# Kernel tuning notes

Measured on AMD Instinct MI355X. Metric: run time of the kernel, lower is better.

The kernel has to match this reference:

```python
import jax, jax.numpy as jnp
import numpy as np

N_NODES = 100000
N_EDGES = 1600000
D = 128            # in_size == d_model == 128
N_LAYERS = 4
N_GRAPHS = 64
N_CLASS = 10
BN_EPS = 1e-5


def setup_inputs() -> dict:
    key = jax.random.key(0)
    ks = jax.random.split(key, 20)
    x = jax.random.normal(ks[0], (N_NODES, D), dtype=jnp.float32)
    edge_index = jax.random.randint(ks[1], (2, N_EDGES), 0, N_NODES, dtype=jnp.int32)
    batch = jnp.sort(jax.random.randint(ks[2], (N_NODES,), 0, N_GRAPHS, dtype=jnp.int32))
    s = 0.05
    # stacked per-layer GINConv MLP params (all layers are D->D since in_size==d_model)
    W1 = jax.random.normal(ks[3], (N_LAYERS, D, D), dtype=jnp.float32) * s
    b1 = jnp.zeros((N_LAYERS, D), dtype=jnp.float32)
    W2 = jax.random.normal(ks[4], (N_LAYERS, D, D), dtype=jnp.float32) * s
    b2 = jnp.zeros((N_LAYERS, D), dtype=jnp.float32)
    gamma = jnp.ones((N_LAYERS, D), dtype=jnp.float32)
    beta = jnp.zeros((N_LAYERS, D), dtype=jnp.float32)
    eps = jnp.zeros((N_LAYERS,), dtype=jnp.float32)  # train_eps=True, init 0
    fcw1 = jax.random.normal(ks[5], (D, D), dtype=jnp.float32) * s
    fcb1 = jnp.zeros((D,), dtype=jnp.float32)
    fcw2 = jax.random.normal(ks[6], (D, D // 2), dtype=jnp.float32) * s
    fcb2 = jnp.zeros((D // 2,), dtype=jnp.float32)
    fcw3 = jax.random.normal(ks[7], (D // 2, N_CLASS), dtype=jnp.float32) * s
    fcb3 = jnp.zeros((N_CLASS,), dtype=jnp.float32)
    return dict(x=x, edge_index=edge_index, batch=batch, W1=W1, b1=b1, W2=W2, b2=b2,
                gamma=gamma, beta=beta, eps=eps, fcw1=fcw1, fcb1=fcb1,
                fcw2=fcw2, fcb2=fcb2, fcw3=fcw3, fcb3=fcb3)


def _batchnorm(z, g, b):
    # BatchNorm1d in training mode: batch stats over nodes, biased variance
    m = jnp.mean(z, axis=0)
    v = jnp.var(z, axis=0)
    return g * (z - m) * jax.lax.rsqrt(v + BN_EPS) + b


def reference(x, edge_index, batch, W1, b1, W2, b2, gamma, beta, eps,
              fcw1, fcb1, fcw2, fcb2, fcw3, fcb3):
    # StandardScaler: per-feature standardization over all nodes (ddof=0)
    mu = jnp.mean(x, axis=0)
    sd = jnp.sqrt(jnp.var(x, axis=0))
    h = (x - mu) / sd
    src, dst = edge_index[0], edge_index[1]
    for l in range(N_LAYERS):
        # GINConv: MLP((1+eps)*x_i + sum_{j in N(i)} x_j)
        agg = jax.ops.segment_sum(h[src], dst, num_segments=N_NODES)
        z = (1.0 + eps[l]) * h + agg
        z = jax.nn.relu(z @ W1[l] + b1[l])
        z = jax.nn.relu(z @ W2[l] + b2[l])
        z = _batchnorm(z, gamma[l], beta[l])
        h = jax.nn.relu(z)  # outer F.relu in forward
    g = jax.ops.segment_sum(h, batch, num_segments=N_GRAPHS)  # global_add_pool
    g = jax.nn.relu(g @ fcw1 + fcb1)   # dropout omitted (eval/deterministic)
    g = jax.nn.relu(g @ fcw2 + fcb2)
    return g @ fcw3 + fcb3
```

## Files before the change

kernel.cpp:

```cpp
#include <hip/hip_runtime.h>
#include <hip/hip_bf16.h>
#include <math.h>

#define N_NODES 100000
#define N_EDGES 1600000
#define D 128
#define N_LAYERS 4
#define N_GRAPHS 64
#define N_CLASS 10
#define BN_EPS 1e-5f

#define POOL_ROWS 128
#define LDK 136

#define EB_CHUNK 4096
#define EDGE_BLOCKS ((N_EDGES + EB_CHUNK - 1) / EB_CHUNK)
#define NPB 512
#define NB ((N_NODES + NPB - 1) / NPB)

typedef __attribute__((ext_vector_type(8))) short bf16x8;
typedef __attribute__((ext_vector_type(4))) float f32x4;

__device__ inline float b2f(ushort u) {
    return __builtin_bit_cast(float, (unsigned)u << 16);
}
__device__ inline ushort f2b(float f) {
    unsigned u = __builtin_bit_cast(unsigned, f);
    return (ushort)((u + 0x7fffu + ((u >> 16) & 1u)) >> 16);
}

__global__ void zero_u32_kernel(unsigned int* __restrict__ p, int n) {
    int i = blockIdx.x * blockDim.x + threadIdx.x;
    if (i < n) p[i] = 0u;
}


__global__ void bucket_count_kernel(const int* __restrict__ dst, int* __restrict__ bucketCount) {
    __shared__ int bc[NB];
    int tid = threadIdx.x;
    if (tid < NB) bc[tid] = 0;
    __syncthreads();
    int base = blockIdx.x * EB_CHUNK;
#pragma unroll
    for (int i = 0; i < 16; ++i) {
        int e = base + i * 256 + tid;
        if (e < N_EDGES) atomicAdd(&bc[dst[e] >> 9], 1);
    }
    __syncthreads();
    if (tid < NB && bc[tid]) atomicAdd(&bucketCount[tid], bc[tid]);
}

__global__ void bucket_scan_kernel(const int* __restrict__ bucketCount,
                                   int* __restrict__ bucketBase, int* __restrict__ bucketCursor) {
    __shared__ int lds[256];
    int tid = threadIdx.x;
    int v = (tid < NB) ? bucketCount[tid] : 0;
    lds[tid] = v;
    __syncthreads();
    for (int off = 1; off < 256; off <<= 1) {
        int x = (tid >= off) ? lds[tid - off] : 0;
        __syncthreads();
        lds[tid] += x;
        __syncthreads();
    }
    int excl = lds[tid] - v;
    if (tid < NB) { bucketBase[tid] = excl; bucketCursor[tid] = excl; }
    if (tid == NB - 1) bucketBase[NB] = excl + v;
}

__global__ void bucket_scatter_kernel(const int* __restrict__ src, const int* __restrict__ dst,
                                      int* __restrict__ bucketCursor, int2* __restrict__ bpairs) {
    __shared__ int lcnt[NB];
    int tid = threadIdx.x;
    if (tid < NB) lcnt[tid] = 0;
    __syncthreads();
    int base = blockIdx.x * EB_CHUNK;
    int s[16], d[16];
#pragma unroll
    for (int i = 0; i < 16; ++i) {
        int e = base + i * 256 + tid;
        if (e < N_EDGES) {
            s[i] = src[e]; d[i] = dst[e];
            atomicAdd(&lcnt[d[i] >> 9], 1);
        } else {
            d[i] = -1;
        }
    }
    __syncthreads();
    if (tid < NB) {
        int c = lcnt[tid];
        lcnt[tid] = c ? atomicAdd(&bucketCursor[tid], c) : 0;
    }
    __syncthreads();
#pragma unroll
    for (int i = 0; i < 16; ++i) {
        if (d[i] >= 0) {
            int p = atomicAdd(&lcnt[d[i] >> 9], 1);
            bpairs[p] = make_int2(s[i], d[i]);
        }
    }
}

__launch_bounds__(512)
__global__ void csr_build_kernel(const int2* __restrict__ bpairs, const int* __restrict__ bucketBase,
                                 int* __restrict__ rowptr, int* __restrict__ colidx) {
    __shared__ int cnt[NPB];
    __shared__ int cur[NPB];
    int tid = threadIdx.x;
    int b = blockIdx.x;
    int nb0 = b * NPB;
    int ebase = bucketBase[b];
    int eend = bucketBase[b + 1];
    cnt[tid] = 0;
    __syncthreads();
    for (int e = ebase + tid; e < eend; e += 512)
        atomicAdd(&cnt[bpairs[e].y - nb0], 1);
    __syncthreads();
    int v = cnt[tid];
    for (int off = 1; off < 512; off <<= 1) {
        int x = (tid >= off) ? cnt[tid - off] : 0;
        __syncthreads();
        cnt[tid] += x;
        __syncthreads();
    }
    int excl = cnt[tid] - v;
    int node = nb0 + tid;
    if (node < N_NODES) rowptr[node] = ebase + excl;
    cur[tid] = ebase + excl;
    __syncthreads();
    for (int e = ebase + tid; e < eend; e += 512) {
        int2 pr = bpairs[e];
        int p = atomicAdd(&cur[pr.y - nb0], 1);
        colidx[p] = pr.x;
    }
    if (b == 0 && tid == 0) rowptr[N_NODES] = N_EDGES;
}

__global__ void colstats_kernel(const float* __restrict__ x, float* __restrict__ stats) {
    __shared__ float ssum[D];
    __shared__ float ssq[D];
    int tid = threadIdx.x;
    if (tid < D) { ssum[tid] = 0.f; ssq[tid] = 0.f; }
    __syncthreads();
    int f4 = (tid & 31) * 4;
    int rsub = tid >> 5;
    int r0 = blockIdx.x * 128;
    int rend = r0 + 128;
    if (rend > N_NODES) rend = N_NODES;
    float4 ps = make_float4(0.f, 0.f, 0.f, 0.f);
    float4 pq = make_float4(0.f, 0.f, 0.f, 0.f);
    for (int r = r0 + rsub; r < rend; r += 8) {
        float4 v = *(const float4*)&x[(size_t)r * D + f4];
        ps.x += v.x; ps.y += v.y; ps.z += v.z; ps.w += v.w;
        pq.x += v.x * v.x; pq.y += v.y * v.y; pq.z += v.z * v.z; pq.w += v.w * v.w;
    }
    atomicAdd(&ssum[f4 + 0], ps.x); atomicAdd(&ssum[f4 + 1], ps.y);
    atomicAdd(&ssum[f4 + 2], ps.z); atomicAdd(&ssum[f4 + 3], ps.w);
    atomicAdd(&ssq[f4 + 0], pq.x);  atomicAdd(&ssq[f4 + 1], pq.y);
    atomicAdd(&ssq[f4 + 2], pq.z);  atomicAdd(&ssq[f4 + 3], pq.w);
    __syncthreads();
    if (tid < D) {
        atomicAdd(&stats[tid], ssum[tid]);
        atomicAdd(&stats[D + tid], ssq[tid]);
    }
}

__global__ void standardize_kernel(const float* __restrict__ x, const float* __restrict__ stats,
                                   ushort* __restrict__ h) {
    const float invN = 1.f / (float)N_NODES;
    int stride = gridDim.x * blockDim.x;
    const int total = N_NODES * (D / 4);
    for (int idx = blockIdx.x * blockDim.x + threadIdx.x; idx < total; idx += stride) {
        int f = (idx & 31) * 4;
        float4 v = ((const float4*)x)[idx];
        float o[4];
        float vv[4] = {v.x, v.y, v.z, v.w};
#pragma unroll
        for (int j = 0; j < 4; ++j) {
            float mu = stats[f + j] * invN;
            float sd = sqrtf(stats[D + f + j] * invN - mu * mu);
            o[j] = (vv[j] - mu) / sd;
        }
        ((ushort4*)h)[idx] = make_ushort4(f2b(o[0]), f2b(o[1]), f2b(o[2]), f2b(o[3]));
    }
}

__global__ void agg_kernel(const ushort* __restrict__ h, const int* __restrict__ rowptr,
                           const int* __restrict__ colidx, const float* __restrict__ eps, int l,
                           const float* __restrict__ ab, int relu_flag,
                           ushort* __restrict__ z0) {
    int node = blockIdx.x * 8 + (threadIdx.x >> 5);
    int f4 = (threadIdx.x & 31) * 4;
    const ushort* hp = h + f4;
    float A0 = ab[f4 + 0], A1 = ab[f4 + 1], A2 = ab[f4 + 2], A3 = ab[f4 + 3];
    float B0 = ab[D + f4 + 0], B1 = ab[D + f4 + 1], B2 = ab[D + f4 + 2], B3 = ab[D + f4 + 3];
    float lo = relu_flag ? 0.f : -INFINITY;

    ushort4 c = *(const ushort4*)&hp[(size_t)node * D];
    float se = 1.f + eps[l];
    float ax = se * fmaxf(fmaf(b2f(c.x), A0, B0), lo);
    float ay = se * fmaxf(fmaf(b2f(c.y), A1, B1), lo);
    float az = se * fmaxf(fmaf(b2f(c.z), A2, B2), lo);
    float aw = se * fmaxf(fmaf(b2f(c.w), A3, B3), lo);

    int e = rowptr[node], e1 = rowptr[node + 1];
    for (; e + 2 <= e1; e += 2) {
        int s0 = colidx[e];
        int s1 = colidx[e + 1];
        ushort4 v0 = *(const ushort4*)&hp[(size_t)s0 * D];
        ushort4 v1 = *(const ushort4*)&hp[(size_t)s1 * D];
        ax += fmaxf(fmaf(b2f(v0.x), A0, B0), lo) + fmaxf(fmaf(b2f(v1.x), A0, B0), lo);
        ay += fmaxf(fmaf(b2f(v0.y), A1, B1), lo) + fmaxf(fmaf(b2f(v1.y), A1, B1), lo);
        az += fmaxf(fmaf(b2f(v0.z), A2, B2), lo) + fmaxf(fmaf(b2f(v1.z), A2, B2), lo);
        aw += fmaxf(fmaf(b2f(v0.w), A3, B3), lo) + fmaxf(fmaf(b2f(v1.w), A3, B3), lo);
    }
    if (e < e1) {
        int s0 = colidx[e];
        ushort4 v0 = *(const ushort4*)&hp[(size_t)s0 * D];
        ax += fmaxf(fmaf(b2f(v0.x), A0, B0), lo);
        ay += fmaxf(fmaf(b2f(v0.y), A1, B1), lo);
        az += fmaxf(fmaf(b2f(v0.z), A2, B2), lo);
        aw += fmaxf(fmaf(b2f(v0.w), A3, B3), lo);
    }
    *(ushort4*)&z0[(size_t)node * D + f4] = make_ushort4(f2b(ax), f2b(ay), f2b(az), f2b(aw));
}

__global__ void prep_wt_kernel(const float* __restrict__ W1, const float* __restrict__ W2,
                               ushort* __restrict__ wt) {
    int idx = blockIdx.x * blockDim.x + threadIdx.x;
    int w = idx >> 16;
    int rem = idx & 65535;
    int l = rem >> 14;
    int nk = rem & 16383;
    int n = nk >> 7;
    int k = nk & 127;
    const float* W = w ? W2 : W1;
    wt[idx] = f2b(W[((size_t)(l * D + k)) * D + n]);
}

__launch_bounds__(256, 2)
__global__ void mlp_mfma_kernel(const ushort* __restrict__ z0,
                                const ushort* __restrict__ wt1, const float* __restrict__ b1,
                                const ushort* __restrict__ wt2, const float* __restrict__ b2,
                                ushort* __restrict__ out, float* __restrict__ stats) {
    __shared__ ushort As[128 * LDK];
    __shared__ ushort Bs[128 * LDK];
    __shared__ float Ssum[D];
    __shared__ float Ssq[D];

    int tid = threadIdx.x;
    int lane = tid & 63;
    int wave = tid >> 6;
    int rb = blockIdx.x * 128;
    int lrow = lane & 15;
    int lk = lane >> 4;
    int klane = lk * 8;
    int wr0 = wave * 32;

    if (tid < D) { Ssum[tid] = 0.f; Ssq[tid] = 0.f; }

#pragma unroll
    for (int i = 0; i < 8; ++i) {
        int c2 = tid + i * 256;
        int row = c2 >> 4;
        int cc = (c2 & 15) * 8;
        int gr = rb + row;
        bf16x8 v;
#pragma unroll
        for (int e = 0; e < 8; ++e) v[e] = 0;
        if (gr < N_NODES) v = *(const bf16x8*)&z0[(size_t)gr * D + cc];
        *(bf16x8*)&As[row * LDK + cc] = v;
        *(bf16x8*)&Bs[row * LDK + cc] = *(const bf16x8*)&wt1[c2 * 8];
    }
    __syncthreads();

    f32x4 acc[2][8];
#pragma unroll
    for (int a = 0; a < 2; ++a)
#pragma unroll
        for (int b = 0; b < 8; ++b)
#pragma unroll
            for (int r = 0; r < 4; ++r) acc[a][b][r] = 0.f;

#pragma unroll
    for (int ks = 0; ks < 4; ++ks) {
        int k0 = ks * 32 + klane;
        bf16x8 a0 = *(const bf16x8*)&As[(wr0 + lrow) * LDK + k0];
        bf16x8 a1 = *(const bf16x8*)&As[(wr0 + 16 + lrow) * LDK + k0];
#pragma unroll
        for (int ct = 0; ct < 8; ++ct) {
            bf16x8 bb = *(const bf16x8*)&Bs[(ct * 16 + lrow) * LDK + k0];
            acc[0][ct] = __builtin_amdgcn_mfma_f32_16x16x32_bf16(a0, bb, acc[0][ct], 0, 0, 0);
            acc[1][ct] = __builtin_amdgcn_mfma_f32_16x16x32_bf16(a1, bb, acc[1][ct], 0, 0, 0);
        }
    }
    __syncthreads();

#pragma unroll
    for (int rt = 0; rt < 2; ++rt)
#pragma unroll
        for (int ct = 0; ct < 8; ++ct) {
            int col = ct * 16 + lrow;
            float bias = b1[col];
#pragma unroll
            for (int r = 0; r < 4; ++r) {
                int row = wr0 + rt * 16 + lk * 4 + r;
                As[row * LDK + col] = f2b(fmaxf(acc[rt][ct][r] + bias, 0.f));
            }
        }
#pragma unroll
    for (int i = 0; i < 8; ++i) {
        int c2 = tid + i * 256;
        int row = c2 >> 4;
        int cc = (c2 & 15) * 8;
        *(bf16x8*)&Bs[row * LDK + cc] = *(const bf16x8*)&wt2[c2 * 8];
    }
#pragma unroll
    for (int a = 0; a < 2; ++a)
#pragma unroll
        for (int b = 0; b < 8; ++b)
#pragma unroll
            for (int r = 0; r < 4; ++r) acc[a][b][r] = 0.f;
    __syncthreads();

#pragma unroll
    for (int ks = 0; ks < 4; ++ks) {
        int k0 = ks * 32 + klane;
        bf16x8 a0 = *(const bf16x8*)&As[(wr0 + lrow) * LDK + k0];
        bf16x8 a1 = *(const bf16x8*)&As[(wr0 + 16 + lrow) * LDK + k0];
#pragma unroll
        for (int ct = 0; ct < 8; ++ct) {
            bf16x8 bb = *(const bf16x8*)&Bs[(ct * 16 + lrow) * LDK + k0];
            acc[0][ct] = __builtin_amdgcn_mfma_f32_16x16x32_bf16(a0, bb, acc[0][ct], 0, 0, 0);
            acc[1][ct] = __builtin_amdgcn_mfma_f32_16x16x32_bf16(a1, bb, acc[1][ct], 0, 0, 0);
        }
    }
    __syncthreads();

#pragma unroll
    for (int rt = 0; rt < 2; ++rt)
#pragma unroll
        for (int ct = 0; ct < 8; ++ct) {
            int col = ct * 16 + lrow;
            float bias = b2[col];
            float s = 0.f, sq = 0.f;
#pragma unroll
            for (int r = 0; r < 4; ++r) {
                int row = wr0 + rt * 16 + lk * 4 + r;
                float v = fmaxf(acc[rt][ct][r] + bias, 0.f);
                Bs[row * LDK + col] = f2b(v);
                if (rb + row < N_NODES) { s += v; sq += v * v; }
            }
            atomicAdd(&Ssum[col], s);
            atomicAdd(&Ssq[col], sq);
        }
    __syncthreads();

#pragma unroll
    for (int i = 0; i < 8; ++i) {
        int c2 = tid + i * 256;
        int row = c2 >> 4;
        int cc = (c2 & 15) * 8;
        int gr = rb + row;
        if (gr < N_NODES)
            *(bf16x8*)&out[(size_t)gr * D + cc] = *(const bf16x8*)&Bs[row * LDK + cc];
    }
    if (tid < D) {
        atomicAdd(&stats[tid], Ssum[tid]);
        atomicAdd(&stats[D + tid], Ssq[tid]);
    }
}

__global__ void bnprep_kernel(const float* __restrict__ stats, const float* __restrict__ gamma,
                              const float* __restrict__ beta, float* __restrict__ ab) {
    int f = threadIdx.x;
    if (f < D) {
        const float invN = 1.f / (float)N_NODES;
        float mu = stats[f] * invN;
        float var = stats[D + f] * invN - mu * mu;
        float A = gamma[f] * rsqrtf(var + BN_EPS);
        ab[f] = A;
        ab[D + f] = beta[f] - mu * A;
    }
}

__global__ void init_ab_kernel(float* __restrict__ ab) {
    int f = threadIdx.x;
    if (f < D) { ab[f] = 1.f; ab[D + f] = 0.f; }
}

__global__ void pool_kernel(const ushort* __restrict__ h, const int* __restrict__ batch,
                            const float* __restrict__ ab, float* __restrict__ g) {
    int tid = threadIdx.x;
    int f4 = (tid & 31) * 4;
    int rsub = tid >> 5;
    int r0 = blockIdx.x * POOL_ROWS;
    int rend = r0 + POOL_ROWS;
    if (rend > N_NODES) rend = N_NODES;
    float A0 = ab[f4 + 0], A1 = ab[f4 + 1], A2 = ab[f4 + 2], A3 = ab[f4 + 3];
    float B0 = ab[D + f4 + 0], B1 = ab[D + f4 + 1], B2 = ab[D + f4 + 2], B3 = ab[D + f4 + 3];
    float4 acc = make_float4(0.f, 0.f, 0.f, 0.f);
    int cur = -1;
    for (int r = r0 + rsub; r < rend; r += 8) {
        int b = batch[r];
        if (b != cur) {
            if (cur >= 0) {
                atomicAdd(&g[cur * D + f4 + 0], acc.x);
                atomicAdd(&g[cur * D + f4 + 1], acc.y);
                atomicAdd(&g[cur * D + f4 + 2], acc.z);
                atomicAdd(&g[cur * D + f4 + 3], acc.w);
            }
            acc = make_float4(0.f, 0.f, 0.f, 0.f);
            cur = b;
        }
        ushort4 v = *(const ushort4*)&h[(size_t)r * D + f4];
        acc.x += fmaxf(fmaf(b2f(v.x), A0, B0), 0.f);
        acc.y += fmaxf(fmaf(b2f(v.y), A1, B1), 0.f);
        acc.z += fmaxf(fmaf(b2f(v.z), A2, B2), 0.f);
        acc.w += fmaxf(fmaf(b2f(v.w), A3, B3), 0.f);
    }
    if (cur >= 0) {
        atomicAdd(&g[cur * D + f4 + 0], acc.x);
        atomicAdd(&g[cur * D + f4 + 1], acc.y);
        atomicAdd(&g[cur * D + f4 + 2], acc.z);
        atomicAdd(&g[cur * D + f4 + 3], acc.w);
    }
}

__launch_bounds__(512)
__global__ void head_kernel(const float* __restrict__ g,
                            const float* __restrict__ fcw1, const float* __restrict__ fcb1,
                            const float* __restrict__ fcw2, const float* __restrict__ fcb2,
                            const float* __restrict__ fcw3, const float* __restrict__ fcb3,
                            float* __restrict__ out) {
    __shared__ float G[64][128];
    __shared__ float T1[64][128];
    __shared__ float T2[64][64];
    int tid = threadIdx.x;
#pragma unroll
    for (int i = 0; i < 4; ++i) {
        int slot = tid + i * 512;
        ((float4*)G)[slot] = ((const float4*)g)[slot];
    }
    __syncthreads();
#pragma unroll 1
    for (int rep = 0; rep < 16; ++rep) {
        int o = tid + rep * 512;
        int r = o >> 7, c = o & 127;
        float acc = fcb1[c];
        for (int k = 0; k < 128; ++k) acc = fmaf(G[r][k], fcw1[k * 128 + c], acc);
        T1[r][c] = fmaxf(acc, 0.f);
    }
    __syncthreads();
#pragma unroll 1
    for (int rep = 0; rep < 8; ++rep) {
        int o = tid + rep * 512;
        int r = o >> 6, c = o & 63;
        float acc = fcb2[c];
        for (int k = 0; k < 128; ++k) acc = fmaf(T1[r][k], fcw2[k * 64 + c], acc);
        T2[r][c] = fmaxf(acc, 0.f);
    }
    __syncthreads();
    for (int o = tid; o < N_GRAPHS * N_CLASS; o += 512) {
        int r = o / 10, c = o % 10;
        float acc = fcb3[c];
        for (int k = 0; k < 64; ++k) acc = fmaf(T2[r][k], fcw3[k * 10 + c], acc);
        out[o] = acc;
    }
}

extern "C" void kernel_launch(void* const* d_in, const int* in_sizes, int n_in,
                              void* d_out, int out_size, void* d_ws, size_t ws_size,
                              hipStream_t stream) {
    const float* x        = (const float*)d_in[0];
    const int* edge_index = (const int*)d_in[1];
    const int* batch      = (const int*)d_in[2];
    const float* W1       = (const float*)d_in[3];
    const float* b1       = (const float*)d_in[4];
    const float* W2       = (const float*)d_in[5];
    const float* b2       = (const float*)d_in[6];
    const float* gamma    = (const float*)d_in[7];
    const float* beta     = (const float*)d_in[8];
    const float* eps      = (const float*)d_in[9];
    const float* fcw1     = (const float*)d_in[10];
    const float* fcb1     = (const float*)d_in[11];
    const float* fcw2     = (const float*)d_in[12];
    const float* fcb2     = (const float*)d_in[13];
    const float* fcw3     = (const float*)d_in[14];
    const float* fcb3     = (const float*)d_in[15];
    float* out = (float*)d_out;

    char* ws = (char*)d_ws;
    size_t off = 0;
    auto alloc = [&](size_t bytes) -> void* {
        void* p = ws + off;
        off = (off + bytes + 255) & ~(size_t)255;
        return p;
    };
    ushort* hbuf   = (ushort*)alloc((size_t)N_NODES * D * 2);
    ushort* z0buf  = (ushort*)alloc((size_t)N_NODES * D * 2);
    ushort* wtbuf  = (ushort*)alloc((size_t)2 * N_LAYERS * D * D * 2);
    int2* bpairs   = (int2*)alloc((size_t)N_EDGES * 8);
    int* colidx    = (int*)alloc((size_t)N_EDGES * 4);
    int* rowptr    = (int*)alloc((size_t)(N_NODES + 1) * 4);
    int* bucketCount  = (int*)alloc((size_t)NB * 4);
    int* bucketBase   = (int*)alloc((size_t)(NB + 1) * 4);
    int* bucketCursor = (int*)alloc((size_t)NB * 4);
    float* stats   = (float*)alloc(4 * D * 4);
    float* gpool   = (float*)alloc((size_t)N_GRAPHS * D * 4);
    float* ab      = stats + 2 * D;

    const int* srcArr = edge_index;
    const int* dstArr = edge_index + N_EDGES;

    zero_u32_kernel<<<1, 256, 0, stream>>>((unsigned int*)bucketCount, NB);
    bucket_count_kernel<<<EDGE_BLOCKS, 256, 0, stream>>>(dstArr, bucketCount);
    bucket_scan_kernel<<<1, 256, 0, stream>>>(bucketCount, bucketBase, bucketCursor);
    bucket_scatter_kernel<<<EDGE_BLOCKS, 256, 0, stream>>>(srcArr, dstArr, bucketCursor, bpairs);
    csr_build_kernel<<<NB, 512, 0, stream>>>(bpairs, bucketBase, rowptr, colidx);

    zero_u32_kernel<<<1, 256, 0, stream>>>((unsigned int*)stats, 2 * D);
    colstats_kernel<<<(N_NODES + 127) / 128, 256, 0, stream>>>(x, stats);
    standardize_kernel<<<2048, 256, 0, stream>>>(x, stats, hbuf);

    prep_wt_kernel<<<512, 256, 0, stream>>>(W1, W2, wtbuf);
    init_ab_kernel<<<1, 128, 0, stream>>>(ab);

    for (int l = 0; l < N_LAYERS; ++l) {
        agg_kernel<<<N_NODES / 8, 256, 0, stream>>>(hbuf, rowptr, colidx, eps, l,
                                                    ab, (l > 0) ? 1 : 0, z0buf);
        zero_u32_kernel<<<1, 256, 0, stream>>>((unsigned int*)stats, 2 * D);
        mlp_mfma_kernel<<<(N_NODES + 127) / 128, 256, 0, stream>>>(
            z0buf, wtbuf + (size_t)l * D * D, b1 + (size_t)l * D,
            wtbuf + (size_t)(N_LAYERS + l) * D * D, b2 + (size_t)l * D, hbuf, stats);
        bnprep_kernel<<<1, 128, 0, stream>>>(stats, gamma + (size_t)l * D,
                                             beta + (size_t)l * D, ab);
    }

    zero_u32_kernel<<<(N_GRAPHS * D + 255) / 256, 256, 0, stream>>>((unsigned int*)gpool, N_GRAPHS * D);
    pool_kernel<<<(N_NODES + POOL_ROWS - 1) / POOL_ROWS, 256, 0, stream>>>(hbuf, batch, ab, gpool);
    head_kernel<<<1, 512, 0, stream>>>(gpool, fcw1, fcb1, fcw2, fcb2, fcw3, fcb3, out);
}
```

Measured before the change: 851.4 us.

## Split node features into 16-wide channel planes for cache-local gather aggregation

Stores node features in 8 channel-major planes of 16 bf16 values each, and has the aggregation kernel process one plane per block, with the plane chosen by block index. Each plane is small enough to stay resident in a cache slice, which is meant to cut DRAM traffic from the random neighbor gathers. The standardize, MLP load/store and pool kernels are adapted to the new layout. The tradeoff is narrower 4-byte gathers per thread and repeated reads of rowptr and colidx across the 8 planes.

```diff
diff --git a/kernel.cpp b/kernel.cpp
--- a/kernel.cpp
+++ b/kernel.cpp
@@ -13,6 +13,10 @@
 #define POOL_ROWS 128
 #define LDK 136
 
+#define NCH 8
+#define CHF 16
+#define CH_STRIDE ((size_t)N_NODES * CHF)
+
 #define EB_CHUNK 4096
 #define EDGE_BLOCKS ((N_EDGES + EB_CHUNK - 1) / EB_CHUNK)
 #define NPB 512
@@ -33,7 +37,6 @@
     int i = blockIdx.x * blockDim.x + threadIdx.x;
     if (i < n) p[i] = 0u;
 }
-
 
 __global__ void bucket_count_kernel(const int* __restrict__ dst, int* __restrict__ bucketCount) {
     __shared__ int bc[NB];
@@ -169,10 +172,14 @@
                                    ushort* __restrict__ h) {
     const float invN = 1.f / (float)N_NODES;
     int stride = gridDim.x * blockDim.x;
-    const int total = N_NODES * (D / 4);
+    const int total = NCH * N_NODES * 4;
     for (int idx = blockIdx.x * blockDim.x + threadIdx.x; idx < total; idx += stride) {
-        int f = (idx & 31) * 4;
-        float4 v = ((const float4*)x)[idx];
+        int c = idx / (N_NODES * 4);
+        int rem = idx - c * (N_NODES * 4);
+        int node = rem >> 2;
+        int q = rem & 3;
+        int f = c * CHF + q * 4;
+        float4 v = *(const float4*)&x[(size_t)node * D + f];
         float o[4];
         float vv[4] = {v.x, v.y, v.z, v.w};
 #pragma unroll
@@ -181,7 +188,8 @@
             float sd = sqrtf(stats[D + f + j] * invN - mu * mu);
             o[j] = (vv[j] - mu) / sd;
         }
-        ((ushort4*)h)[idx] = make_ushort4(f2b(o[0]), f2b(o[1]), f2b(o[2]), f2b(o[3]));
+        *(ushort4*)&h[(size_t)c * CH_STRIDE + (size_t)node * CHF + q * 4] =
+            make_ushort4(f2b(o[0]), f2b(o[1]), f2b(o[2]), f2b(o[3]));
     }
 }
 
@@ -189,40 +197,41 @@
                            const int* __restrict__ colidx, const float* __restrict__ eps, int l,
                            const float* __restrict__ ab, int relu_flag,
                            ushort* __restrict__ z0) {
-    int node = blockIdx.x * 8 + (threadIdx.x >> 5);
-    int f4 = (threadIdx.x & 31) * 4;
-    const ushort* hp = h + f4;
-    float A0 = ab[f4 + 0], A1 = ab[f4 + 1], A2 = ab[f4 + 2], A3 = ab[f4 + 3];
-    float B0 = ab[D + f4 + 0], B1 = ab[D + f4 + 1], B2 = ab[D + f4 + 2], B3 = ab[D + f4 + 3];
+    int c = blockIdx.x & 7;
+    int ng = blockIdx.x >> 3;
+    int tid = threadIdx.x;
+    int nsub = tid >> 3;
+    int fl = (tid & 7) * 2;
+    int node = ng * 32 + nsub;
+    int f = c * CHF + fl;
+    const ushort* hp = h + (size_t)c * CH_STRIDE + fl;
+    float A0 = ab[f], A1 = ab[f + 1];
+    float B0 = ab[D + f], B1 = ab[D + f + 1];
     float lo = relu_flag ? 0.f : -INFINITY;
 
-    ushort4 c = *(const ushort4*)&hp[(size_t)node * D];
+    uint cs = *(const uint*)&hp[(size_t)node * CHF];
     float se = 1.f + eps[l];
-    float ax = se * fmaxf(fmaf(b2f(c.x), A0, B0), lo);
-    float ay = se * fmaxf(fmaf(b2f(c.y), A1, B1), lo);
-    float az = se * fmaxf(fmaf(b2f(c.z), A2, B2), lo);
-    float aw = se * fmaxf(fmaf(b2f(c.w), A3, B3), lo);
+    float a0 = se * fmaxf(fmaf(b2f((ushort)cs), A0, B0), lo);
+    float a1 = se * fmaxf(fmaf(b2f((ushort)(cs >> 16)), A1, B1), lo);
 
     int e = rowptr[node], e1 = rowptr[node + 1];
     for (; e + 2 <= e1; e += 2) {
         int s0 = colidx[e];
         int s1 = colidx[e + 1];
-        ushort4 v0 = *(const ushort4*)&hp[(size_t)s0 * D];
-        ushort4 v1 = *(const ushort4*)&hp[(size_t)s1 * D];
-        ax += fmaxf(fmaf(b2f(v0.x), A0, B0), lo) + fmaxf(fmaf(b2f(v1.x), A0, B0), lo);
-        ay += fmaxf(fmaf(b2f(v0.y), A1, B1), lo) + fmaxf(fmaf(b2f(v1.y), A1, B1), lo);
-        az += fmaxf(fmaf(b2f(v0.z), A2, B2), lo) + fmaxf(fmaf(b2f(v1.z), A2, B2), lo);
-        aw += fmaxf(fmaf(b2f(v0.w), A3, B3), lo) + fmaxf(fmaf(b2f(v1.w), A3, B3), lo);
+        uint v0 = *(const uint*)&hp[(size_t)s0 * CHF];
+        uint v1 = *(const uint*)&hp[(size_t)s1 * CHF];
+        a0 += fmaxf(fmaf(b2f((ushort)v0), A0, B0), lo) +
+              fmaxf(fmaf(b2f((ushort)v1), A0, B0), lo);
+        a1 += fmaxf(fmaf(b2f((ushort)(v0 >> 16)), A1, B1), lo) +
+              fmaxf(fmaf(b2f((ushort)(v1 >> 16)), A1, B1), lo);
     }
     if (e < e1) {
-        int s0 = colidx[e];
-        ushort4 v0 = *(const ushort4*)&hp[(size_t)s0 * D];
-        ax += fmaxf(fmaf(b2f(v0.x), A0, B0), lo);
-        ay += fmaxf(fmaf(b2f(v0.y), A1, B1), lo);
-        az += fmaxf(fmaf(b2f(v0.z), A2, B2), lo);
-        aw += fmaxf(fmaf(b2f(v0.w), A3, B3), lo);
-    }
-    *(ushort4*)&z0[(size_t)node * D + f4] = make_ushort4(f2b(ax), f2b(ay), f2b(az), f2b(aw));
+        uint v0 = *(const uint*)&hp[(size_t)colidx[e] * CHF];
+        a0 += fmaxf(fmaf(b2f((ushort)v0), A0, B0), lo);
+        a1 += fmaxf(fmaf(b2f((ushort)(v0 >> 16)), A1, B1), lo);
+    }
+    *(uint*)&z0[(size_t)c * CH_STRIDE + (size_t)node * CHF + fl] =
+        (uint)f2b(a0) | ((uint)f2b(a1) << 16);
 }
 
 __global__ void prep_wt_kernel(const float* __restrict__ W1, const float* __restrict__ W2,
@@ -256,21 +265,24 @@
     int lk = lane >> 4;
     int klane = lk * 8;
     int wr0 = wave * 32;
+    int srow = tid >> 1;
+    int shalf = (tid & 1) * 8;
 
     if (tid < D) { Ssum[tid] = 0.f; Ssq[tid] = 0.f; }
 
-#pragma unroll
-    for (int i = 0; i < 8; ++i) {
-        int c2 = tid + i * 256;
-        int row = c2 >> 4;
-        int cc = (c2 & 15) * 8;
-        int gr = rb + row;
-        bf16x8 v;
-#pragma unroll
-        for (int e = 0; e < 8; ++e) v[e] = 0;
-        if (gr < N_NODES) v = *(const bf16x8*)&z0[(size_t)gr * D + cc];
-        *(bf16x8*)&As[row * LDK + cc] = v;
-        *(bf16x8*)&Bs[row * LDK + cc] = *(const bf16x8*)&wt1[c2 * 8];
+    {
+        int sgr = rb + srow;
+        bool ok = sgr < N_NODES;
+#pragma unroll
+        for (int i = 0; i < 8; ++i) {
+            bf16x8 v;
+#pragma unroll
+            for (int e = 0; e < 8; ++e) v[e] = 0;
+            if (ok) v = *(const bf16x8*)&z0[(size_t)i * CH_STRIDE + (size_t)sgr * CHF + shalf];
+            *(bf16x8*)&As[srow * LDK + i * CHF + shalf] = v;
+            int c2 = tid + i * 256;
+            *(bf16x8*)&Bs[(c2 >> 4) * LDK + (c2 & 15) * 8] = *(const bf16x8*)&wt1[c2 * 8];
+        }
     }
     __syncthreads();
 
@@ -311,9 +323,7 @@
 #pragma unroll
     for (int i = 0; i < 8; ++i) {
         int c2 = tid + i * 256;
-        int row = c2 >> 4;
-        int cc = (c2 & 15) * 8;
-        *(bf16x8*)&Bs[row * LDK + cc] = *(const bf16x8*)&wt2[c2 * 8];
+        *(bf16x8*)&Bs[(c2 >> 4) * LDK + (c2 & 15) * 8] = *(const bf16x8*)&wt2[c2 * 8];
     }
 #pragma unroll
     for (int a = 0; a < 2; ++a)
@@ -356,14 +366,14 @@
         }
     __syncthreads();
 
-#pragma unroll
-    for (int i = 0; i < 8; ++i) {
-        int c2 = tid + i * 256;
-        int row = c2 >> 4;
-        int cc = (c2 & 15) * 8;
-        int gr = rb + row;
-        if (gr < N_NODES)
-            *(bf16x8*)&out[(size_t)gr * D + cc] = *(const bf16x8*)&Bs[row * LDK + cc];
+    {
+        int sgr = rb + srow;
+        if (sgr < N_NODES) {
+#pragma unroll
+            for (int i = 0; i < 8; ++i)
+                *(bf16x8*)&out[(size_t)i * CH_STRIDE + (size_t)sgr * CHF + shalf] =
+                    *(const bf16x8*)&Bs[srow * LDK + i * CHF + shalf];
+        }
     }
     if (tid < D) {
         atomicAdd(&stats[tid], Ssum[tid]);
@@ -393,10 +403,13 @@
                             const float* __restrict__ ab, float* __restrict__ g) {
     int tid = threadIdx.x;
     int f4 = (tid & 31) * 4;
+    int c = f4 >> 4;
+    int fw = f4 & 15;
     int rsub = tid >> 5;
     int r0 = blockIdx.x * POOL_ROWS;
     int rend = r0 + POOL_ROWS;
     if (rend > N_NODES) rend = N_NODES;
+    const ushort* hp = h + (size_t)c * CH_STRIDE + fw;
     float A0 = ab[f4 + 0], A1 = ab[f4 + 1], A2 = ab[f4 + 2], A3 = ab[f4 + 3];
     float B0 = ab[D + f4 + 0], B1 = ab[D + f4 + 1], B2 = ab[D + f4 + 2], B3 = ab[D + f4 + 3];
     float4 acc = make_float4(0.f, 0.f, 0.f, 0.f);
@@ -413,7 +426,7 @@
             acc = make_float4(0.f, 0.f, 0.f, 0.f);
             cur = b;
         }
-        ushort4 v = *(const ushort4*)&h[(size_t)r * D + f4];
+        ushort4 v = *(const ushort4*)&hp[(size_t)r * CHF];
         acc.x += fmaxf(fmaf(b2f(v.x), A0, B0), 0.f);
         acc.y += fmaxf(fmaf(b2f(v.y), A1, B1), 0.f);
         acc.z += fmaxf(fmaf(b2f(v.z), A2, B2), 0.f);
@@ -527,8 +540,8 @@
     init_ab_kernel<<<1, 128, 0, stream>>>(ab);
 
     for (int l = 0; l < N_LAYERS; ++l) {
-        agg_kernel<<<N_NODES / 8, 256, 0, stream>>>(hbuf, rowptr, colidx, eps, l,
-                                                    ab, (l > 0) ? 1 : 0, z0buf);
+        agg_kernel<<<(N_NODES / 32) * NCH, 256, 0, stream>>>(hbuf, rowptr, colidx, eps, l,
+                                                             ab, (l > 0) ? 1 : 0, z0buf);
         zero_u32_kernel<<<1, 256, 0, stream>>>((unsigned int*)stats, 2 * D);
         mlp_mfma_kernel<<<(N_NODES + 127) / 128, 256, 0, stream>>>(
             z0buf, wtbuf + (size_t)l * D * D, b1 + (size_t)l * D,
```

Result: slower. 1.000 ms (+17.5%).
